# Kernel tuning notes

Hardware: AMD Instinct MI355X
Metric: run time of the kernel (lower is better)

Reference implementation:

```python
import jax, jax.numpy as jnp
import numpy as np

N = 100_000      # nodes
E0 = 1_600_000   # raw edges (avg degree 16)
D = 128          # input_dim
H = 8            # heads
C = 16           # out_channels per head (feat_dim // n_head)
F = H * C        # feat_dim = 128
NCLS = 40
SLOPE = 0.2      # LeakyReLU negative_slope


def setup_inputs() -> dict:
    key = jax.random.key(0)
    ks = jax.random.split(key, 16)

    def glorot(k, shape, fan_in, fan_out):
        lim = np.sqrt(6.0 / (fan_in + fan_out))
        return jax.random.uniform(k, shape, jnp.float32, -lim, lim)

    inp = {
        "x": jax.random.normal(ks[0], (N, D), jnp.float32),
        "edge_index": jax.random.randint(ks[1], (2, E0), 0, N, jnp.int32),
        "edge_weight": jax.random.uniform(ks[2], (E0,), jnp.float32),
        # layer 1 params
        "W1": glorot(ks[3], (D, F), D, F),
        "att_l1": glorot(ks[4], (1, H, C), C, C),
        "att_r1": glorot(ks[5], (1, H, C), C, C),
        "b1": jnp.zeros((F,), jnp.float32),
        # layer 2 params
        "W2": glorot(ks[6], (F, F), F, F),
        "att_l2": glorot(ks[7], (1, H, C), C, C),
        "att_r2": glorot(ks[8], (1, H, C), C, C),
        "b2": jnp.zeros((F,), jnp.float32),
        # classifier
        "Wc": glorot(ks[9], (F, NCLS), F, NCLS),
        "bc": jnp.zeros((NCLS,), jnp.float32),
    }
    return inp


def _gat_layer(x, src, dst, mask, W, att_l, att_r, b):
    # x: [N, Din] -> h: [N, H, C]
    h = (x @ W).reshape(-1, H, C)
    al = jnp.sum(h * att_l, axis=-1)   # [N, H]
    ar = jnp.sum(h * att_r, axis=-1)   # [N, H]
    # per-edge score: alpha_j(src) + alpha_i(dst), LeakyReLU
    e = al[src] + ar[dst]              # [E, H]
    e = jnp.where(e > 0, e, SLOPE * e)
    # destination-grouped stable softmax (masked self-loop dups excluded)
    m = jax.ops.segment_max(e, dst, num_segments=N)
    m = jnp.where(jnp.isfinite(m), m, 0.0)
    ex = jnp.exp(e - m[dst]) * mask[:, None]
    denom = jax.ops.segment_sum(ex, dst, num_segments=N)
    alpha = ex / jnp.maximum(denom[dst], 1e-16)   # [E, H]
    # message = x_j * alpha, scatter-add to dst
    msg = h[src] * alpha[..., None]               # [E, H, C]
    out = jax.ops.segment_sum(msg, dst, num_segments=N)
    return out.reshape(-1, F) + b                 # concat heads + bias


def _augment(edge_index, dtype):
    # remove self-loops (via mask) then add one self-loop per node
    src0, dst0 = edge_index[0], edge_index[1]
    loop = jnp.arange(N, dtype=edge_index.dtype)
    src = jnp.concatenate([src0, loop])
    dst = jnp.concatenate([dst0, loop])
    mask = jnp.concatenate([(src0 != dst0).astype(dtype), jnp.ones((N,), dtype)])
    return src, dst, mask


def reference(x, edge_index, edge_weight, W1, att_l1, att_r1, b1,
              W2, att_l2, att_r2, b2, Wc, bc):
    # edge_weight is accepted but unused, matching the torch forward
    src, dst, mask = _augment(edge_index, x.dtype)
    h = _gat_layer(x, src, dst, mask, W1, att_l1, att_r1, b1)
    h = jax.nn.elu(h)
    h = _gat_layer(h, src, dst, mask, W2, att_l2, att_r2, b2)
    h = jax.nn.elu(h)
    # eval mode: dropout is identity
    return h @ Wc + bc
```

## Files before the change

kernel.cpp:

```cpp
#include <hip/hip_runtime.h>
#include <hip/hip_bf16.h>
#include <math.h>

#define NN 100000
#define E_RAW 1600000
#define E_TOT 1700000
#define HEADS 8
#define CH 16
#define FDIM 128
#define NCLS 40
#define SLOPE 0.2f

__device__ __forceinline__ float elu1(float v) { return v > 0.f ? v : expm1f(v); }

__device__ __forceinline__ unsigned short f2bf(float f) {
    unsigned int u = __float_as_uint(f);
    u += 0x7fffu + ((u >> 16) & 1u);
    return (unsigned short)(u >> 16);
}

__global__ __launch_bounds__(256) void gemm128_alar(const float* __restrict__ X,
                                                    const float* __restrict__ Wm,
                                                    const float* __restrict__ attl,
                                                    const float* __restrict__ attr,
                                                    unsigned short* __restrict__ Hb,
                                                    float* __restrict__ AL,
                                                    float* __restrict__ AR) {
    __shared__ float xs[32][132];
    const int cpair = threadIdx.x & 63;
    const int rgrp  = threadIdx.x >> 6;
    const int row0 = blockIdx.x << 5;
    for (int i = threadIdx.x; i < 32 * 128; i += 256) {
        int r = i >> 7, k = i & 127;
        xs[r][k] = X[(size_t)(row0 + r) * 128 + k];
    }
    __syncthreads();
    float acc[8][2];
    #pragma unroll
    for (int r = 0; r < 8; ++r) { acc[r][0] = 0.f; acc[r][1] = 0.f; }
    const float* wp = Wm + 2 * cpair;
    for (int k = 0; k < 128; k += 4) {
        float w00 = wp[(k+0)*128], w01 = wp[(k+0)*128 + 1];
        float w10 = wp[(k+1)*128], w11 = wp[(k+1)*128 + 1];
        float w20 = wp[(k+2)*128], w21 = wp[(k+2)*128 + 1];
        float w30 = wp[(k+3)*128], w31 = wp[(k+3)*128 + 1];
        #pragma unroll
        for (int r = 0; r < 8; ++r) {
            const float4 xv = *(const float4*)&xs[rgrp*8 + r][k];
            acc[r][0] = fmaf(xv.w, w30, fmaf(xv.z, w20, fmaf(xv.y, w10, fmaf(xv.x, w00, acc[r][0]))));
            acc[r][1] = fmaf(xv.w, w31, fmaf(xv.z, w21, fmaf(xv.y, w11, fmaf(xv.x, w01, acc[r][1]))));
        }
    }
    #pragma unroll
    for (int r = 0; r < 8; ++r) {
        ushort2 p; p.x = f2bf(acc[r][0]); p.y = f2bf(acc[r][1]);
        *(ushort2*)&Hb[(size_t)(row0 + rgrp*8 + r) * 128 + 2*cpair] = p;
    }

    const float lw0 = attl[2*cpair], lw1 = attl[2*cpair+1];
    const float rw0 = attr[2*cpair], rw1 = attr[2*cpair+1];
    const int hd = cpair >> 3;
    #pragma unroll
    for (int r = 0; r < 8; ++r) {
        float pl = acc[r][0]*lw0 + acc[r][1]*lw1;
        float pr = acc[r][0]*rw0 + acc[r][1]*rw1;
        #pragma unroll
        for (int off = 1; off < 8; off <<= 1) {
            pl += __shfl_xor(pl, off);
            pr += __shfl_xor(pr, off);
        }
        if ((cpair & 7) == 0) {
            int nd = row0 + rgrp*8 + r;
            AL[nd*8 + hd] = pl;
            AR[nd*8 + hd] = pr;
        }
    }
}

__global__ __launch_bounds__(256) void csr_init_cnt(int* __restrict__ cnt) {
    int i = blockIdx.x * 256 + threadIdx.x;
    if (i < NN) cnt[i] = 1;
}

__global__ __launch_bounds__(256) void csr_hist(const int* __restrict__ dst_a,
                                                int* __restrict__ cnt) {
    int e = blockIdx.x * 256 + threadIdx.x;
    if (e < E_RAW) atomicAdd(&cnt[dst_a[e]], 1);
}

__global__ __launch_bounds__(256) void scan_block(const int* __restrict__ cnt,
                                                  int* __restrict__ part,
                                                  int* __restrict__ bsum) {
    __shared__ int s[256];
    int i = blockIdx.x * 256 + threadIdx.x;
    int v = (i < NN) ? cnt[i] : 0;
    s[threadIdx.x] = v;
    __syncthreads();
    for (int off = 1; off < 256; off <<= 1) {
        int t = (threadIdx.x >= off) ? s[threadIdx.x - off] : 0;
        __syncthreads();
        s[threadIdx.x] += t;
        __syncthreads();
    }
    if (i < NN) part[i] = s[threadIdx.x] - v;
    if (threadIdx.x == 255) bsum[blockIdx.x] = s[255];
}

__global__ __launch_bounds__(512) void scan_partials(int* __restrict__ bsum, int nb) {
    __shared__ int s[512];
    int v = (threadIdx.x < nb) ? bsum[threadIdx.x] : 0;
    s[threadIdx.x] = v;
    __syncthreads();
    for (int off = 1; off < 512; off <<= 1) {
        int t = (threadIdx.x >= off) ? s[threadIdx.x - off] : 0;
        __syncthreads();
        s[threadIdx.x] += t;
        __syncthreads();
    }
    if (threadIdx.x < nb) bsum[threadIdx.x] = s[threadIdx.x] - v;
}

__global__ __launch_bounds__(256) void scan_add(const int* __restrict__ part,
                                                const int* __restrict__ bsum,
                                                int* __restrict__ roff,
                                                int* __restrict__ rpos) {
    int i = blockIdx.x * 256 + threadIdx.x;
    if (i < NN) {
        int v = part[i] + bsum[blockIdx.x];
        roff[i] = v; rpos[i] = v;
    }
    if (i == NN) roff[NN] = E_TOT;
}

__global__ __launch_bounds__(256) void csr_scatter(const int* __restrict__ src_a,
                                                   const int* __restrict__ dst_a,
                                                   int* __restrict__ rpos,
                                                   int* __restrict__ csr) {
    int e = blockIdx.x * 256 + threadIdx.x;
    if (e >= E_TOT) return;
    int s, d, flag;
    if (e < E_RAW) { s = src_a[e]; d = dst_a[e]; flag = (s == d); }
    else           { s = d = e - E_RAW; flag = 0; }
    int pos = atomicAdd(&rpos[d], 1);
    csr[pos] = s | (flag << 31);
}

__global__ __launch_bounds__(256) void gat_fused(const int* __restrict__ roff,
                                                 const int* __restrict__ csr,
                                                 const float* __restrict__ AL,
                                                 const float* __restrict__ AR,
                                                 const unsigned short* __restrict__ Hb,
                                                 const float* __restrict__ bias,
                                                 float* __restrict__ Out) {
    const int lane = threadIdx.x & 63;
    const int n = blockIdx.x * 4 + (threadIdx.x >> 6);
    const int r0 = roff[n], r1 = roff[n + 1];

    const int hd = lane >> 3;
    const int t  = lane & 7;
    const float ard = AR[n * 8 + hd];
    float m = -3e38f, den = 0.f;
    for (int j = r0 + t; j < r1; j += 8) {
        int sw = csr[j];
        int s = sw & 0x7fffffff;
        float ev = AL[s * 8 + hd] + ard;
        ev = fmaxf(ev, SLOPE * ev);
        float mn = fmaxf(m, ev);
        float add = (sw >= 0) ? __expf(ev - mn) : 0.f;
        den = fmaf(den, __expf(m - mn), add);
        m = mn;
    }
    #pragma unroll
    for (int off = 1; off < 8; off <<= 1) {
        float m2 = __shfl_xor(m, off), d2 = __shfl_xor(den, off);
        float mn = fmaxf(m, m2);
        den = den * __expf(m - mn) + d2 * __expf(m2 - mn);
        m = mn;
    }
    const float S = m + __logf(fmaxf(den, 1e-16f));

    const int ef = lane >> 3;
    const int fl = lane & 7;
    const float S_b  = __shfl(S,   fl * 8);
    const float ar_b = __shfl(ard, fl * 8);
    float4 a0 = make_float4(0.f,0.f,0.f,0.f), a1 = a0, a2 = a0, a3 = a0;
    for (int j = r0; j < r1; j += 8) {
        int jj = j + ef;
        if (jj < r1) {
            int sw = csr[jj];
            int s = sw & 0x7fffffff;
            float ev = AL[s * 8 + fl] + ar_b;
            ev = fmaxf(ev, SLOPE * ev);
            float alpha = (sw >= 0) ? __expf(ev - S_b) : 0.f;
            const unsigned short* hp = Hb + (size_t)s * 128 + fl * 16;
            const uint4 q0 = *(const uint4*)hp;
            const uint4 q1 = *(const uint4*)(hp + 8);
            a0.x = fmaf(__uint_as_float(q0.x << 16),          alpha, a0.x);
            a0.y = fmaf(__uint_as_float(q0.x & 0xffff0000u),  alpha, a0.y);
            a0.z = fmaf(__uint_as_float(q0.y << 16),          alpha, a0.z);
            a0.w = fmaf(__uint_as_float(q0.y & 0xffff0000u),  alpha, a0.w);
            a1.x = fmaf(__uint_as_float(q0.z << 16),          alpha, a1.x);
            a1.y = fmaf(__uint_as_float(q0.z & 0xffff0000u),  alpha, a1.y);
            a1.z = fmaf(__uint_as_float(q0.w << 16),          alpha, a1.z);
            a1.w = fmaf(__uint_as_float(q0.w & 0xffff0000u),  alpha, a1.w);
            a2.x = fmaf(__uint_as_float(q1.x << 16),          alpha, a2.x);
            a2.y = fmaf(__uint_as_float(q1.x & 0xffff0000u),  alpha, a2.y);
            a2.z = fmaf(__uint_as_float(q1.y << 16),          alpha, a2.z);
            a2.w = fmaf(__uint_as_float(q1.y & 0xffff0000u),  alpha, a2.w);
            a3.x = fmaf(__uint_as_float(q1.z << 16),          alpha, a3.x);
            a3.y = fmaf(__uint_as_float(q1.z & 0xffff0000u),  alpha, a3.y);
            a3.z = fmaf(__uint_as_float(q1.w << 16),          alpha, a3.z);
            a3.w = fmaf(__uint_as_float(q1.w & 0xffff0000u),  alpha, a3.w);
        }
    }
    #pragma unroll
    for (int off = 8; off < 64; off <<= 1) {
        a0.x += __shfl_xor(a0.x, off); a0.y += __shfl_xor(a0.y, off);
        a0.z += __shfl_xor(a0.z, off); a0.w += __shfl_xor(a0.w, off);
        a1.x += __shfl_xor(a1.x, off); a1.y += __shfl_xor(a1.y, off);
        a1.z += __shfl_xor(a1.z, off); a1.w += __shfl_xor(a1.w, off);
        a2.x += __shfl_xor(a2.x, off); a2.y += __shfl_xor(a2.y, off);
        a2.z += __shfl_xor(a2.z, off); a2.w += __shfl_xor(a2.w, off);
        a3.x += __shfl_xor(a3.x, off); a3.y += __shfl_xor(a3.y, off);
        a3.z += __shfl_xor(a3.z, off); a3.w += __shfl_xor(a3.w, off);
    }
    if (lane < 8) {
        const float4* bp = (const float4*)(bias + lane * 16);
        float4 b0 = bp[0], b1 = bp[1], b2 = bp[2], b3 = bp[3];
        a0.x = elu1(a0.x + b0.x); a0.y = elu1(a0.y + b0.y);
        a0.z = elu1(a0.z + b0.z); a0.w = elu1(a0.w + b0.w);
        a1.x = elu1(a1.x + b1.x); a1.y = elu1(a1.y + b1.y);
        a1.z = elu1(a1.z + b1.z); a1.w = elu1(a1.w + b1.w);
        a2.x = elu1(a2.x + b2.x); a2.y = elu1(a2.y + b2.y);
        a2.z = elu1(a2.z + b2.z); a2.w = elu1(a2.w + b2.w);
        a3.x = elu1(a3.x + b3.x); a3.y = elu1(a3.y + b3.y);
        a3.z = elu1(a3.z + b3.z); a3.w = elu1(a3.w + b3.w);
        float4* op = (float4*)(Out + (size_t)n * 128 + lane * 16);
        op[0] = a0; op[1] = a1; op[2] = a2; op[3] = a3;
    }
}

__global__ __launch_bounds__(256) void classifier(const float* __restrict__ X,
                                                  const float* __restrict__ Wc,
                                                  const float* __restrict__ bc,
                                                  float* __restrict__ Out) {
    __shared__ float ws[128 * NCLS];
    __shared__ float xs[32][132];
    for (int i = threadIdx.x; i < 128 * NCLS; i += 256) ws[i] = Wc[i];
    const int row0 = blockIdx.x << 5;
    for (int i = threadIdx.x; i < 32 * 128; i += 256) {
        int r = i >> 7, k = i & 127;
        xs[r][k] = X[(size_t)(row0 + r) * 128 + k];
    }
    __syncthreads();
    const int r  = threadIdx.x >> 3;
    const int c0 = (threadIdx.x & 7) * 5;
    float acc[5] = {0.f,0.f,0.f,0.f,0.f};
    for (int k = 0; k < 128; ++k) {
        float xv = xs[r][k];
        #pragma unroll
        for (int j = 0; j < 5; ++j)
            acc[j] = fmaf(xv, ws[k * NCLS + c0 + j], acc[j]);
    }
    #pragma unroll
    for (int j = 0; j < 5; ++j)
        Out[(size_t)(row0 + r) * NCLS + c0 + j] = acc[j] + bc[c0 + j];
}

extern "C" void kernel_launch(void* const* d_in, const int* in_sizes, int n_in,
                              void* d_out, int out_size, void* d_ws, size_t ws_size,
                              hipStream_t stream) {
    const float* x    = (const float*)d_in[0];
    const int*   ei   = (const int*)  d_in[1];
    const float* W1   = (const float*)d_in[3];
    const float* al1  = (const float*)d_in[4];
    const float* ar1  = (const float*)d_in[5];
    const float* b1   = (const float*)d_in[6];
    const float* W2   = (const float*)d_in[7];
    const float* al2  = (const float*)d_in[8];
    const float* ar2  = (const float*)d_in[9];
    const float* b2   = (const float*)d_in[10];
    const float* Wc   = (const float*)d_in[11];
    const float* bc   = (const float*)d_in[12];
    float* out = (float*)d_out;

    const int* src = ei;
    const int* dst = ei + E_RAW;

    char* ws = (char*)d_ws;
    unsigned short* hb = (unsigned short*)(ws);
    float* acc  = (float*)(ws + 51200000UL);
    float* AL   = (float*)(ws + 102400000UL);
    float* AR   = (float*)(ws + 105600000UL);
    int*   csr  = (int*)  (ws + 108800000UL);
    int*   cnt  = (int*)  (ws + 115600000UL);
    int*   roff = (int*)  (ws + 116000000UL);
    int*   rpos = (int*)  (ws + 116400004UL);
    int*   part = (int*)  (ws + 116800004UL);
    int*   bsum = (int*)  (ws + 117200004UL);

    const int NB_N    = (NN + 255) / 256;
    const int gRaw    = (E_RAW + 255) / 256;
    const int gTot    = (E_TOT + 255) / 256;
    const int gRows32 = NN / 32;
    const int gGat    = NN / 4;

    csr_init_cnt<<<NB_N, 256, 0, stream>>>(cnt);
    csr_hist<<<gRaw, 256, 0, stream>>>(dst, cnt);
    scan_block<<<NB_N, 256, 0, stream>>>(cnt, part, bsum);
    scan_partials<<<1, 512, 0, stream>>>(bsum, NB_N);
    scan_add<<<NB_N, 256, 0, stream>>>(part, bsum, roff, rpos);
    csr_scatter<<<gTot, 256, 0, stream>>>(src, dst, rpos, csr);

    gemm128_alar<<<gRows32, 256, 0, stream>>>(x, W1, al1, ar1, hb, AL, AR);
    gat_fused<<<gGat, 256, 0, stream>>>(roff, csr, AL, AR, hb, b1, acc);

    gemm128_alar<<<gRows32, 256, 0, stream>>>(acc, W2, al2, ar2, hb, AL, AR);
    gat_fused<<<gGat, 256, 0, stream>>>(roff, csr, AL, AR, hb, b2, acc);

    classifier<<<gRows32, 256, 0, stream>>>(acc, Wc, bc, out);
}
```

Measured before the change: 713.9 us.

## Replace scalar FP32 GEMM with split-bf16 MFMA GEMM for both GAT layers

The node feature transform now uses bf16 MFMA 16x16x32 instructions, with a three-product hi/lo split of both X and W to approximate FP32 accuracy. A new prep kernel transposes W1 and W2 and splits them into hi and lo bf16 halves once per call. The epilogue still writes bf16 H and computes the per-head attention logits with 16-lane shuffles. The aim is to cut the ALU-bound FP32 GEMM cost. In exchange it adds the split arithmetic, an extra small kernel, and B fragments read straight from global memory without LDS staging.

```diff
diff --git a/kernel.cpp b/kernel.cpp
--- a/kernel.cpp
+++ b/kernel.cpp
@@ -11,6 +11,9 @@
 #define NCLS 40
 #define SLOPE 0.2f
 
+typedef short bf16x8 __attribute__((ext_vector_type(8)));
+typedef float f32x4  __attribute__((ext_vector_type(4)));
+
 __device__ __forceinline__ float elu1(float v) { return v > 0.f ? v : expm1f(v); }
 
 __device__ __forceinline__ unsigned short f2bf(float f) {
@@ -18,61 +21,93 @@
     u += 0x7fffu + ((u >> 16) & 1u);
     return (unsigned short)(u >> 16);
 }
-
-__global__ __launch_bounds__(256) void gemm128_alar(const float* __restrict__ X,
-                                                    const float* __restrict__ Wm,
-                                                    const float* __restrict__ attl,
-                                                    const float* __restrict__ attr,
-                                                    unsigned short* __restrict__ Hb,
-                                                    float* __restrict__ AL,
-                                                    float* __restrict__ AR) {
-    __shared__ float xs[32][132];
-    const int cpair = threadIdx.x & 63;
-    const int rgrp  = threadIdx.x >> 6;
-    const int row0 = blockIdx.x << 5;
-    for (int i = threadIdx.x; i < 32 * 128; i += 256) {
-        int r = i >> 7, k = i & 127;
-        xs[r][k] = X[(size_t)(row0 + r) * 128 + k];
-    }
-    __syncthreads();
-    float acc[8][2];
-    #pragma unroll
-    for (int r = 0; r < 8; ++r) { acc[r][0] = 0.f; acc[r][1] = 0.f; }
-    const float* wp = Wm + 2 * cpair;
-    for (int k = 0; k < 128; k += 4) {
-        float w00 = wp[(k+0)*128], w01 = wp[(k+0)*128 + 1];
-        float w10 = wp[(k+1)*128], w11 = wp[(k+1)*128 + 1];
-        float w20 = wp[(k+2)*128], w21 = wp[(k+2)*128 + 1];
-        float w30 = wp[(k+3)*128], w31 = wp[(k+3)*128 + 1];
+__device__ __forceinline__ float bf2f(unsigned short h) {
+    return __uint_as_float((unsigned int)h << 16);
+}
+
+__global__ __launch_bounds__(256) void prep_w(const float* __restrict__ W1,
+                                              const float* __restrict__ W2,
+                                              unsigned short* __restrict__ whi1,
+                                              unsigned short* __restrict__ wlo1,
+                                              unsigned short* __restrict__ whi2,
+                                              unsigned short* __restrict__ wlo2) {
+    int t = blockIdx.x * 256 + threadIdx.x;
+    const float* W = (t < 16384) ? W1 : W2;
+    unsigned short* hi = (t < 16384) ? whi1 : whi2;
+    unsigned short* lo = (t < 16384) ? wlo1 : wlo2;
+    int e = t & 16383;
+    int k = e & 127, n = e >> 7;
+    float v = W[k * 128 + n];
+    unsigned short h = f2bf(v);
+    float r = v - bf2f(h);
+    hi[e] = h; lo[e] = f2bf(r);
+}
+
+__global__ __launch_bounds__(256) void gemm_mfma(const float* __restrict__ X,
+                                                 const unsigned short* __restrict__ Whi,
+                                                 const unsigned short* __restrict__ Wlo,
+                                                 const float* __restrict__ attl,
+                                                 const float* __restrict__ attr,
+                                                 unsigned short* __restrict__ Hb,
+                                                 float* __restrict__ AL,
+                                                 float* __restrict__ AR) {
+    const int lane = threadIdx.x & 63;
+    const int w    = threadIdx.x >> 6;
+    const int m16  = lane & 15;
+    const int koct = lane >> 4;
+    const int rowA = blockIdx.x * 64 + w * 16 + m16;
+    const int rowAc = rowA < NN ? rowA : NN - 1;
+
+    f32x4 acc[8];
+    #pragma unroll
+    for (int c = 0; c < 8; ++c) acc[c] = (f32x4){0.f, 0.f, 0.f, 0.f};
+
+    #pragma unroll
+    for (int ks = 0; ks < 4; ++ks) {
+        const int k0 = ks * 32;
+        const float* xp = X + (size_t)rowAc * 128 + k0 + koct * 8;
+        float xv[8];
+        *(float4*)&xv[0] = *(const float4*)xp;
+        *(float4*)&xv[4] = *(const float4*)(xp + 4);
+        bf16x8 ahi, alo;
         #pragma unroll
-        for (int r = 0; r < 8; ++r) {
-            const float4 xv = *(const float4*)&xs[rgrp*8 + r][k];
-            acc[r][0] = fmaf(xv.w, w30, fmaf(xv.z, w20, fmaf(xv.y, w10, fmaf(xv.x, w00, acc[r][0]))));
-            acc[r][1] = fmaf(xv.w, w31, fmaf(xv.z, w21, fmaf(xv.y, w11, fmaf(xv.x, w01, acc[r][1]))));
+        for (int j = 0; j < 8; ++j) {
+            unsigned short h = f2bf(xv[j]);
+            ahi[j] = (short)h;
+            alo[j] = (short)f2bf(xv[j] - bf2f(h));
         }
-    }
-    #pragma unroll
-    for (int r = 0; r < 8; ++r) {
-        ushort2 p; p.x = f2bf(acc[r][0]); p.y = f2bf(acc[r][1]);
-        *(ushort2*)&Hb[(size_t)(row0 + rgrp*8 + r) * 128 + 2*cpair] = p;
-    }
-
-    const float lw0 = attl[2*cpair], lw1 = attl[2*cpair+1];
-    const float rw0 = attr[2*cpair], rw1 = attr[2*cpair+1];
-    const int hd = cpair >> 3;
-    #pragma unroll
-    for (int r = 0; r < 8; ++r) {
-        float pl = acc[r][0]*lw0 + acc[r][1]*lw1;
-        float pr = acc[r][0]*rw0 + acc[r][1]*rw1;
         #pragma unroll
-        for (int off = 1; off < 8; off <<= 1) {
-            pl += __shfl_xor(pl, off);
-            pr += __shfl_xor(pr, off);
+        for (int cf = 0; cf < 8; ++cf) {
+            const size_t boff = (size_t)(cf * 16 + m16) * 128 + k0 + koct * 8;
+            bf16x8 bhi = *(const bf16x8*)(Whi + boff);
+            bf16x8 blo = *(const bf16x8*)(Wlo + boff);
+            acc[cf] = __builtin_amdgcn_mfma_f32_16x16x32_bf16(ahi, bhi, acc[cf], 0, 0, 0);
+            acc[cf] = __builtin_amdgcn_mfma_f32_16x16x32_bf16(alo, bhi, acc[cf], 0, 0, 0);
+            acc[cf] = __builtin_amdgcn_mfma_f32_16x16x32_bf16(ahi, blo, acc[cf], 0, 0, 0);
         }
-        if ((cpair & 7) == 0) {
-            int nd = row0 + rgrp*8 + r;
-            AL[nd*8 + hd] = pl;
-            AR[nd*8 + hd] = pr;
+    }
+
+    const int orow0 = blockIdx.x * 64 + w * 16 + koct * 4;
+    #pragma unroll
+    for (int cf = 0; cf < 8; ++cf) {
+        const float lwv = attl[cf * 16 + m16];
+        const float rwv = attr[cf * 16 + m16];
+        #pragma unroll
+        for (int r = 0; r < 4; ++r) {
+            const int orow = orow0 + r;
+            if (orow < NN)
+                Hb[(size_t)orow * 128 + cf * 16 + m16] = f2bf(acc[cf][r]);
+            float pl = acc[cf][r] * lwv;
+            float pr = acc[cf][r] * rwv;
+            #pragma unroll
+            for (int off = 1; off < 16; off <<= 1) {
+                pl += __shfl_xor(pl, off);
+                pr += __shfl_xor(pr, off);
+            }
+            if (m16 == 0 && orow < NN) {
+                AL[orow * 8 + cf] = pl;
+                AR[orow * 8 + cf] = pr;
+            }
         }
     }
 }
@@ -289,6 +324,10 @@
 
     char* ws = (char*)d_ws;
     unsigned short* hb = (unsigned short*)(ws);
+    unsigned short* whi1 = (unsigned short*)(ws + 25600000UL);
+    unsigned short* wlo1 = (unsigned short*)(ws + 25632768UL);
+    unsigned short* whi2 = (unsigned short*)(ws + 25665536UL);
+    unsigned short* wlo2 = (unsigned short*)(ws + 25698304UL);
     float* acc  = (float*)(ws + 51200000UL);
     float* AL   = (float*)(ws + 102400000UL);
     float* AR   = (float*)(ws + 105600000UL);
@@ -303,7 +342,10 @@
     const int gRaw    = (E_RAW + 255) / 256;
     const int gTot    = (E_TOT + 255) / 256;
     const int gRows32 = NN / 32;
+    const int gGemm   = (NN + 63) / 64;
     const int gGat    = NN / 4;
+
+    prep_w<<<128, 256, 0, stream>>>(W1, W2, whi1, wlo1, whi2, wlo2);
 
     csr_init_cnt<<<NB_N, 256, 0, stream>>>(cnt);
     csr_hist<<<gRaw, 256, 0, stream>>>(dst, cnt);
@@ -312,10 +354,10 @@
     scan_add<<<NB_N, 256, 0, stream>>>(part, bsum, roff, rpos);
     csr_scatter<<<gTot, 256, 0, stream>>>(src, dst, rpos, csr);
 
-    gemm128_alar<<<gRows32, 256, 0, stream>>>(x, W1, al1, ar1, hb, AL, AR);
+    gemm_mfma<<<gGemm, 256, 0, stream>>>(x, whi1, wlo1, al1, ar1, hb, AL, AR);
     gat_fused<<<gGat, 256, 0, stream>>>(roff, csr, AL, AR, hb, b1, acc);
 
-    gemm128_alar<<<gRows32, 256, 0, stream>>>(acc, W2, al2, ar2, hb, AL, AR);
+    gemm_mfma<<<gGemm, 256, 0, stream>>>(acc, whi2, wlo2, al2, ar2, hb, AL, AR);
     gat_fused<<<gGat, 256, 0, stream>>>(roff, csr, AL, AR, hb, b2, acc);
 
     classifier<<<gRows32, 256, 0, stream>>>(acc, Wc, bc, out);
```

Result: slower. 739.1 us (+3.5%).
